# Kernel optimization log

Hardware: AMD Instinct MI355X
Metric: run time of the kernel (lower is better)

The kernel has to match this reference:

```python
import jax, jax.numpy as jnp
import numpy as np

B, T, C, H = 2, 2048, 1024, 16
HD = C // H  # head dim = 64


def setup_inputs() -> dict:
    key = jax.random.key(0)
    ks = jax.random.split(key, 5)
    scale = 0.02
    return {
        "x": jax.random.normal(ks[0], (B, T, C), dtype=jnp.float32),
        "W_attn": jax.random.normal(ks[1], (C, 3 * C), dtype=jnp.float32) * scale,
        "b_attn": jax.random.normal(ks[2], (3 * C,), dtype=jnp.float32) * scale,
        "W_proj": jax.random.normal(ks[3], (C, C), dtype=jnp.float32) * scale,
        "b_proj": jax.random.normal(ks[4], (C,), dtype=jnp.float32) * scale,
    }


def reference(x, W_attn, b_attn, W_proj, b_proj):
    Bd, Td, Cd = x.shape
    qkv = x @ W_attn + b_attn                      # [B,T,3C]
    q, k, v = jnp.split(qkv, 3, axis=-1)           # each [B,T,C]
    # [B,T,C] -> [B,H,T,HD]
    def heads(t):
        return t.reshape(Bd, Td, H, HD).transpose(0, 2, 1, 3)
    q, k, v = heads(q), heads(k), heads(v)
    att = jnp.einsum('bhqd,bhkd->bhqk', q, k) * (1.0 / np.sqrt(HD))
    causal = jnp.tril(jnp.ones((Td, Td), dtype=bool))
    att = jnp.where(causal[None, None, :, :], att, -jnp.inf)
    att = jax.nn.softmax(att, axis=-1)
    y = jnp.einsum('bhqk,bhkd->bhqd', att, v)      # [B,H,T,HD]
    y = y.transpose(0, 2, 1, 3).reshape(Bd, Td, Cd)
    return y @ W_proj + b_proj
```

## Files before the change

### kernel.cpp

```cpp
#include <hip/hip_runtime.h>
#include <hip/hip_bf16.h>


typedef __attribute__((ext_vector_type(8))) __bf16 bf16x8;
typedef __attribute__((ext_vector_type(8))) short short8;
typedef __attribute__((ext_vector_type(4))) short short4v;
typedef __attribute__((ext_vector_type(4))) float floatx4;

__device__ __forceinline__ unsigned short f2b(float f) {
    unsigned int x = __float_as_uint(f);
    x += 0x7fffu + ((x >> 16) & 1u);
    return (unsigned short)(x >> 16);
}
__device__ __forceinline__ unsigned short f2b_trunc(float f) {
    return (unsigned short)(__float_as_uint(f) >> 16);
}
__device__ __forceinline__ void gld16(const void* g, void* l) {
    __builtin_amdgcn_global_load_lds((const __attribute__((address_space(1))) void*)g,
                                     (__attribute__((address_space(3))) void*)l, 16, 0, 0);
}

__global__ __launch_bounds__(256) void cvt_k(
    const float* __restrict__ in, unsigned short* __restrict__ out, int n)
{
    int i = (blockIdx.x * 256 + threadIdx.x) << 3;
    if (i >= n) return;
    const float4 a = *(const float4*)(in + i);
    const float4 b = *(const float4*)(in + i + 4);
    short8 v;
    v[0] = (short)f2b(a.x); v[1] = (short)f2b(a.y);
    v[2] = (short)f2b(a.z); v[3] = (short)f2b(a.w);
    v[4] = (short)f2b(b.x); v[5] = (short)f2b(b.y);
    v[6] = (short)f2b(b.z); v[7] = (short)f2b(b.w);
    *(short8*)(out + i) = v;
}

__global__ __launch_bounds__(256) void transpose_cvt_k(
    const float* __restrict__ in, unsigned short* __restrict__ out,
    int R, int Cc)
{
    __shared__ unsigned short tl[64][72];
    const int t = threadIdx.x;
    const int r0 = blockIdx.y * 64, c0 = blockIdx.x * 64;
#pragma unroll
    for (int it = 0; it < 2; ++it) {
        int idx = it * 256 + t, r = idx >> 3, c8 = (idx & 7) << 3;
        const float* p = in + (size_t)(r0 + r) * Cc + c0 + c8;
        const float4 a = *(const float4*)p;
        const float4 b = *(const float4*)(p + 4);
        tl[r][c8 + 0] = f2b(a.x); tl[r][c8 + 1] = f2b(a.y);
        tl[r][c8 + 2] = f2b(a.z); tl[r][c8 + 3] = f2b(a.w);
        tl[r][c8 + 4] = f2b(b.x); tl[r][c8 + 5] = f2b(b.y);
        tl[r][c8 + 6] = f2b(b.z); tl[r][c8 + 7] = f2b(b.w);
    }
    __syncthreads();
#pragma unroll
    for (int it = 0; it < 2; ++it) {
        int idx = it * 256 + t, rr = idx >> 3, c8 = (idx & 7) << 3;
        short8 v;
#pragma unroll
        for (int i = 0; i < 8; ++i) v[i] = (short)tl[c8 + i][rr];
        *(short8*)(out + (size_t)(c0 + rr) * R + r0 + c8) = v;
    }
}

__global__ __launch_bounds__(256) void gemm_qkv(
    const unsigned short* __restrict__ A,
    const unsigned short* __restrict__ BT,
    const float* __restrict__ bias,
    unsigned short* __restrict__ outqk,
    unsigned short* __restrict__ outvt)
{
    __shared__ unsigned short Ald[128][32];
    __shared__ unsigned short Bld[128][32];
    __shared__ __align__(16) unsigned short Esc[128 * 72];

    const int t = threadIdx.x;
    const int w = t >> 6, lane = t & 63, l15 = lane & 15, quad = lane >> 4;
    const int wr = w >> 1, wc = w & 1;
    const int m0 = blockIdx.y * 128, n0 = blockIdx.x * 128;
    const int K = 1024;

    float bia[4];
#pragma unroll
    for (int j = 0; j < 4; ++j) bia[j] = bias[n0 + wc * 64 + j * 16 + l15];

    floatx4 acc[4][4];
#pragma unroll
    for (int i = 0; i < 4; ++i)
#pragma unroll
        for (int j = 0; j < 4; ++j) acc[i][j] = (floatx4)0.f;

    const int row_s = t >> 2, kg_s = (t & 3) << 3;
    for (int k0 = 0; k0 < K; k0 += 32) {
        __syncthreads();
#pragma unroll
        for (int c = 0; c < 2; ++c) {
            int row = c * 64 + row_s;
            gld16(A  + (size_t)(m0 + row) * K + k0 + kg_s, &Ald[0][0] + (size_t)(c * 256 + w * 64) * 8);
            gld16(BT + (size_t)(n0 + row) * K + k0 + kg_s, &Bld[0][0] + (size_t)(c * 256 + w * 64) * 8);
        }
        __syncthreads();

        bf16x8 af[4], bfr[4];
#pragma unroll
        for (int i = 0; i < 4; ++i) af[i] = *(const bf16x8*)&Ald[wr * 64 + i * 16 + l15][quad * 8];
#pragma unroll
        for (int j = 0; j < 4; ++j) bfr[j] = *(const bf16x8*)&Bld[wc * 64 + j * 16 + l15][quad * 8];
#pragma unroll
        for (int i = 0; i < 4; ++i)
#pragma unroll
            for (int j = 0; j < 4; ++j)
                acc[i][j] = __builtin_amdgcn_mfma_f32_16x16x32_bf16(af[i], bfr[j], acc[i][j], 0, 0, 0);
    }

    const int bb = m0 >> 11, tbase = m0 & 2047;
    if (n0 < 2048) {
        for (int cf = 0; cf < 2; ++cf) {
            __syncthreads();
            if (wc == cf) {
#pragma unroll
                for (int i = 0; i < 4; ++i)
#pragma unroll
                    for (int j = 0; j < 4; ++j)
#pragma unroll
                        for (int r = 0; r < 4; ++r)
                            Esc[(wr * 64 + i * 16 + quad * 4 + r) * 72 + j * 16 + l15] =
                                f2b(acc[i][j][r] + bia[j]);
            }
            __syncthreads();
            const int fb = n0 + cf * 64;
            const int which = fb >> 10, h = (fb & 1023) >> 6;
            const int row = t >> 1, co = (t & 1) << 5;
            const unsigned short* src = Esc + row * 72 + co;
            unsigned short* dst = outqk + (size_t)which * 4194304
                + (((size_t)(bb * 16 + h) * 2048 + tbase + row) * 64 + co);
#pragma unroll
            for (int u = 0; u < 4; ++u)
                *(short8*)(dst + u * 8) = *(const short8*)(src + u * 8);
        }
    } else {
        const int hb = (n0 & 1023) >> 6;
        for (int hf = 0; hf < 2; ++hf) {
            __syncthreads();
            if (wr == hf) {
#pragma unroll
                for (int i = 0; i < 4; ++i)
#pragma unroll
                    for (int j = 0; j < 4; ++j) {
                        short4v pk;
#pragma unroll
                        for (int r = 0; r < 4; ++r) pk[r] = (short)f2b(acc[i][j][r] + bia[j]);
                        *(short4v*)&Esc[(wc * 64 + j * 16 + l15) * 72 + i * 16 + quad * 4] = pk;
                    }
            }
            __syncthreads();
            const int dl = t >> 1, co = (t & 1) << 5;
            const int h = hb + (dl >> 6), d = dl & 63;
            const unsigned short* src = Esc + dl * 72 + co;
            unsigned short* dst = outvt
                + (((size_t)(bb * 16 + h) * 64 + d) * 2048 + tbase + hf * 64 + co);
#pragma unroll
            for (int u = 0; u < 4; ++u)
                *(short8*)(dst + u * 8) = *(const short8*)(src + u * 8);
        }
    }
}

__global__ __launch_bounds__(256) void gemm_proj(
    const unsigned short* __restrict__ A,
    const unsigned short* __restrict__ BT,
    const float* __restrict__ bias,
    float* __restrict__ outf)
{
    __shared__ unsigned short Ald[128][32];
    __shared__ unsigned short Bld[64][32];
    __shared__ __align__(16) float Ef[32 * 68];

    const int t = threadIdx.x;
    const int w = t >> 6, lane = t & 63, l15 = lane & 15, quad = lane >> 4;
    const int m0 = blockIdx.y * 128, n0 = blockIdx.x * 64;
    const int K = 1024, N = 1024;

    float bia[4];
#pragma unroll
    for (int j = 0; j < 4; ++j) bia[j] = bias[n0 + j * 16 + l15];

    floatx4 acc[2][4];
#pragma unroll
    for (int i = 0; i < 2; ++i)
#pragma unroll
        for (int j = 0; j < 4; ++j) acc[i][j] = (floatx4)0.f;

    const int row_s = t >> 2, kg_s = (t & 3) << 3;
    for (int k0 = 0; k0 < K; k0 += 32) {
        __syncthreads();
#pragma unroll
        for (int c = 0; c < 2; ++c)
            gld16(A + (size_t)(m0 + c * 64 + row_s) * K + k0 + kg_s,
                  &Ald[0][0] + (size_t)(c * 256 + w * 64) * 8);
        gld16(BT + (size_t)(n0 + row_s) * K + k0 + kg_s,
              &Bld[0][0] + (size_t)(w * 64) * 8);
        __syncthreads();

        bf16x8 af[2], bfr[4];
#pragma unroll
        for (int i = 0; i < 2; ++i) af[i] = *(const bf16x8*)&Ald[w * 32 + i * 16 + l15][quad * 8];
#pragma unroll
        for (int j = 0; j < 4; ++j) bfr[j] = *(const bf16x8*)&Bld[j * 16 + l15][quad * 8];
#pragma unroll
        for (int i = 0; i < 2; ++i)
#pragma unroll
            for (int j = 0; j < 4; ++j)
                acc[i][j] = __builtin_amdgcn_mfma_f32_16x16x32_bf16(af[i], bfr[j], acc[i][j], 0, 0, 0);
    }

    for (int qf = 0; qf < 4; ++qf) {
        __syncthreads();
        if (w == qf) {
#pragma unroll
            for (int i = 0; i < 2; ++i)
#pragma unroll
                for (int j = 0; j < 4; ++j)
#pragma unroll
                    for (int r = 0; r < 4; ++r)
                        Ef[(i * 16 + quad * 4 + r) * 68 + j * 16 + l15] = acc[i][j][r] + bia[j];
        }
        __syncthreads();
        const int row = t >> 3, co = (t & 7) << 3;
        const float* src = Ef + row * 68 + co;
        float* dst = outf + (size_t)(m0 + qf * 32 + row) * N + n0 + co;
#pragma unroll
        for (int u = 0; u < 2; ++u)
            *(float4*)(dst + u * 4) = *(const float4*)(src + u * 4);
    }
}

__global__ __launch_bounds__(256) void attn_k(
    const unsigned short* __restrict__ qg,
    const unsigned short* __restrict__ kg,
    const unsigned short* __restrict__ vt,
    unsigned short* __restrict__ y)
{
    __shared__ unsigned short Kb[2][64][64];
    __shared__ unsigned short Vb[2][64][64];
    __shared__ unsigned short Pld[4][16][72];

    const int t = threadIdx.x, w = t >> 6, lane = t & 63;
    const int l15 = lane & 15, quad = lane >> 4;
    const int bh = blockIdx.x >> 4, p = blockIdx.x & 15;
    const int b = bh >> 4, h = bh & 15;
    const float SC = 0.18033688011112042f;

    bf16x8 ones;
#pragma unroll
    for (int i = 0; i < 8; ++i) ones[i] = (__bf16)1.0f;

    const int r_s = t >> 3;
    const int g_s = t & 7;

#pragma unroll 1
    for (int hv = 0; hv < 2; ++hv) {
        const int qt = hv ? (31 - p) : p;
        const int qbase = qt * 64;

        bf16x8 qa[2];
        {
            const unsigned short* qrow = qg + ((size_t)bh * 2048 + qbase + w * 16 + l15) * 64;
            qa[0] = *(const bf16x8*)(qrow + quad * 8);
            qa[1] = *(const bf16x8*)(qrow + 32 + quad * 8);
        }

        floatx4 O[4];
#pragma unroll
        for (int j = 0; j < 4; ++j) O[j] = (floatx4)0.f;
        floatx4 lacc = (floatx4)0.f;

        __syncthreads();
        {
#pragma unroll
            for (int c = 0; c < 2; ++c) {
                int r = c * 32 + r_s;
                int cg = (g_s ^ (r & 7)) << 3;
                gld16(kg + ((size_t)bh * 2048 + r) * 64 + cg,
                      &Kb[0][0][0] + (size_t)(c * 256 + w * 64) * 8);
                gld16(vt + ((size_t)bh * 64 + r) * 2048 + cg,
                      &Vb[0][0][0] + (size_t)(c * 256 + w * 64) * 8);
            }
        }

#pragma unroll 1
        for (int kt = 0; kt <= qt; ++kt) {
            __syncthreads();
            const int cur = kt & 1;
            if (kt < qt) {
                const int kbase = (kt + 1) * 64, nxt = cur ^ 1;
#pragma unroll
                for (int c = 0; c < 2; ++c) {
                    int r = c * 32 + r_s;
                    int cg = (g_s ^ (r & 7)) << 3;
                    gld16(kg + ((size_t)bh * 2048 + kbase + r) * 64 + cg,
                          &Kb[nxt][0][0] + (size_t)(c * 256 + w * 64) * 8);
                    gld16(vt + ((size_t)bh * 64 + r) * 2048 + kbase + cg,
                          &Vb[nxt][0][0] + (size_t)(c * 256 + w * 64) * 8);
                }
            }

            floatx4 sv[4];
#pragma unroll
            for (int jn = 0; jn < 4; ++jn) sv[jn] = (floatx4)0.f;
#pragma unroll
            for (int kk = 0; kk < 2; ++kk) {
#pragma unroll
                for (int jn = 0; jn < 4; ++jn) {
                    bf16x8 bfr = *(const bf16x8*)&Kb[cur][jn * 16 + l15][((kk * 4 + quad) ^ (l15 & 7)) << 3];
                    sv[jn] = __builtin_amdgcn_mfma_f32_16x16x32_bf16(qa[kk], bfr, sv[jn], 0, 0, 0);
                }
            }

            if (kt == qt) {
#pragma unroll
                for (int jn = 0; jn < 4; ++jn) {
                    int key = jn * 16 + l15;
#pragma unroll
                    for (int r = 0; r < 4; ++r) {
                        int qr = w * 16 + quad * 4 + r;
                        float s = (key > qr) ? -1e30f : sv[jn][r];
                        sv[jn][r] = exp2f(s * SC);
                    }
                }
            } else {
#pragma unroll
                for (int jn = 0; jn < 4; ++jn)
#pragma unroll
                    for (int r = 0; r < 4; ++r) sv[jn][r] = exp2f(sv[jn][r] * SC);
            }

#pragma unroll
            for (int jn = 0; jn < 4; ++jn)
#pragma unroll
                for (int r = 0; r < 4; ++r)
                    Pld[w][quad * 4 + r][jn * 16 + l15] = f2b_trunc(sv[jn][r]);
            __builtin_amdgcn_wave_barrier();
            __builtin_amdgcn_s_waitcnt(0xc07f);
            __builtin_amdgcn_wave_barrier();

#pragma unroll
            for (int kk = 0; kk < 2; ++kk) {
                bf16x8 pa = *(const bf16x8*)&Pld[w][l15][kk * 32 + quad * 8];
                lacc = __builtin_amdgcn_mfma_f32_16x16x32_bf16(pa, ones, lacc, 0, 0, 0);
#pragma unroll
                for (int jd = 0; jd < 4; ++jd) {
                    bf16x8 vb = *(const bf16x8*)&Vb[cur][jd * 16 + l15][((kk * 4 + quad) ^ (l15 & 7)) << 3];
                    O[jd] = __builtin_amdgcn_mfma_f32_16x16x32_bf16(pa, vb, O[jd], 0, 0, 0);
                }
            }
        }

#pragma unroll
        for (int r = 0; r < 4; ++r) {
            float inv = 1.f / lacc[r];
            int tt = qbase + w * 16 + quad * 4 + r;
#pragma unroll
            for (int jd = 0; jd < 4; ++jd) {
                int c = h * 64 + jd * 16 + l15;
                y[((size_t)b * 2048 + tt) * 1024 + c] = f2b(O[jd][r] * inv);
            }
        }
    }
}

extern "C" void kernel_launch(void* const* d_in, const int* in_sizes, int n_in,
                              void* d_out, int out_size, void* d_ws, size_t ws_size,
                              hipStream_t stream) {
    const float* x      = (const float*)d_in[0];
    const float* W_attn = (const float*)d_in[1];
    const float* b_attn = (const float*)d_in[2];
    const float* W_proj = (const float*)d_in[3];
    const float* b_proj = (const float*)d_in[4];
    float* out = (float*)d_out;

    char* ws = (char*)d_ws;
    unsigned short* qk  = (unsigned short*)(ws);
    unsigned short* vtb = (unsigned short*)(ws + 16777216);
    unsigned short* y   = (unsigned short*)(ws + 25165824);
    unsigned short* xb  = (unsigned short*)(ws + 33554432);
    unsigned short* WTa = (unsigned short*)(ws + 41943040);
    unsigned short* WTp = (unsigned short*)(ws + 48234496);

    cvt_k<<<2048, 256, 0, stream>>>(x, xb, 4194304);
    transpose_cvt_k<<<dim3(48, 16), 256, 0, stream>>>(W_attn, WTa, 1024, 3072);
    transpose_cvt_k<<<dim3(16, 16), 256, 0, stream>>>(W_proj, WTp, 1024, 1024);
    gemm_qkv<<<dim3(24, 32), 256, 0, stream>>>(xb, WTa, b_attn, qk, vtb);
    attn_k<<<512, 256, 0, stream>>>(qk, qk + 4194304, vtb, y);
    gemm_proj<<<dim3(16, 32), 256, 0, stream>>>(y, WTp, b_proj, out);
}
```

Before: 209.3 us.

## Double-buffer LDS in both GEMMs and widen projection tile to 128x128

Both GEMM kernels now use two LDS buffers. The next K-slice is fetched with global_load_lds while MFMAs run on the current one, and one of the two barriers per iteration is dropped. The projection GEMM also moves from 128x64 to 128x128 tiles with a 2x2 wave layout, so each block does more reuse per load but the grid shrinks to 256 blocks. The epilogue scratch is aliased onto the double buffer to limit LDS use. The main risk is the single-barrier scheme: it relies on the async LDS writes having completed before the next barrier without an explicit vmcnt wait.

```diff
diff --git a/kernel.cpp b/kernel.cpp
--- a/kernel.cpp
+++ b/kernel.cpp
@@ -71,9 +71,8 @@
     unsigned short* __restrict__ outqk,
     unsigned short* __restrict__ outvt)
 {
-    __shared__ unsigned short Ald[128][32];
-    __shared__ unsigned short Bld[128][32];
-    __shared__ __align__(16) unsigned short Esc[128 * 72];
+    __shared__ __align__(16) unsigned short SM[2][2][128][32];
+    unsigned short* Esc = &SM[0][0][0][0];
 
     const int t = threadIdx.x;
     const int w = t >> 6, lane = t & 63, l15 = lane & 15, quad = lane >> 4;
@@ -92,21 +91,32 @@
         for (int j = 0; j < 4; ++j) acc[i][j] = (floatx4)0.f;
 
     const int row_s = t >> 2, kg_s = (t & 3) << 3;
-    for (int k0 = 0; k0 < K; k0 += 32) {
+    const unsigned short* gA = A  + (size_t)(m0 + row_s) * K + kg_s;
+    const unsigned short* gB = BT + (size_t)(n0 + row_s) * K + kg_s;
+    const int ldst = (w * 64) * 8;
+
+#pragma unroll
+    for (int c = 0; c < 2; ++c) {
+        gld16(gA + (size_t)c * 64 * K, &SM[0][0][0][0] + c * 2048 + ldst);
+        gld16(gB + (size_t)c * 64 * K, &SM[0][1][0][0] + c * 2048 + ldst);
+    }
+
+    for (int it = 0; it < 32; ++it) {
         __syncthreads();
-#pragma unroll
-        for (int c = 0; c < 2; ++c) {
-            int row = c * 64 + row_s;
-            gld16(A  + (size_t)(m0 + row) * K + k0 + kg_s, &Ald[0][0] + (size_t)(c * 256 + w * 64) * 8);
-            gld16(BT + (size_t)(n0 + row) * K + k0 + kg_s, &Bld[0][0] + (size_t)(c * 256 + w * 64) * 8);
-        }
-        __syncthreads();
-
+        const int cur = it & 1;
+        if (it < 31) {
+            const int k0 = (it + 1) * 32;
+#pragma unroll
+            for (int c = 0; c < 2; ++c) {
+                gld16(gA + (size_t)c * 64 * K + k0, &SM[cur ^ 1][0][0][0] + c * 2048 + ldst);
+                gld16(gB + (size_t)c * 64 * K + k0, &SM[cur ^ 1][1][0][0] + c * 2048 + ldst);
+            }
+        }
         bf16x8 af[4], bfr[4];
 #pragma unroll
-        for (int i = 0; i < 4; ++i) af[i] = *(const bf16x8*)&Ald[wr * 64 + i * 16 + l15][quad * 8];
-#pragma unroll
-        for (int j = 0; j < 4; ++j) bfr[j] = *(const bf16x8*)&Bld[wc * 64 + j * 16 + l15][quad * 8];
+        for (int i = 0; i < 4; ++i) af[i] = *(const bf16x8*)&SM[cur][0][wr * 64 + i * 16 + l15][quad * 8];
+#pragma unroll
+        for (int j = 0; j < 4; ++j) bfr[j] = *(const bf16x8*)&SM[cur][1][wc * 64 + j * 16 + l15][quad * 8];
 #pragma unroll
         for (int i = 0; i < 4; ++i)
 #pragma unroll
@@ -173,43 +183,54 @@
     const float* __restrict__ bias,
     float* __restrict__ outf)
 {
-    __shared__ unsigned short Ald[128][32];
-    __shared__ unsigned short Bld[64][32];
-    __shared__ __align__(16) float Ef[32 * 68];
+    __shared__ __align__(16) unsigned short SM[2][2][128][32];
+    float* Ef = (float*)&SM[0][0][0][0];
 
     const int t = threadIdx.x;
     const int w = t >> 6, lane = t & 63, l15 = lane & 15, quad = lane >> 4;
-    const int m0 = blockIdx.y * 128, n0 = blockIdx.x * 64;
+    const int wr = w >> 1, wc = w & 1;
+    const int m0 = blockIdx.y * 128, n0 = blockIdx.x * 128;
     const int K = 1024, N = 1024;
 
     float bia[4];
 #pragma unroll
-    for (int j = 0; j < 4; ++j) bia[j] = bias[n0 + j * 16 + l15];
-
-    floatx4 acc[2][4];
-#pragma unroll
-    for (int i = 0; i < 2; ++i)
+    for (int j = 0; j < 4; ++j) bia[j] = bias[n0 + wc * 64 + j * 16 + l15];
+
+    floatx4 acc[4][4];
+#pragma unroll
+    for (int i = 0; i < 4; ++i)
 #pragma unroll
         for (int j = 0; j < 4; ++j) acc[i][j] = (floatx4)0.f;
 
     const int row_s = t >> 2, kg_s = (t & 3) << 3;
-    for (int k0 = 0; k0 < K; k0 += 32) {
+    const unsigned short* gA = A  + (size_t)(m0 + row_s) * K + kg_s;
+    const unsigned short* gB = BT + (size_t)(n0 + row_s) * K + kg_s;
+    const int ldst = (w * 64) * 8;
+
+#pragma unroll
+    for (int c = 0; c < 2; ++c) {
+        gld16(gA + (size_t)c * 64 * K, &SM[0][0][0][0] + c * 2048 + ldst);
+        gld16(gB + (size_t)c * 64 * K, &SM[0][1][0][0] + c * 2048 + ldst);
+    }
+
+    for (int it = 0; it < 32; ++it) {
         __syncthreads();
-#pragma unroll
-        for (int c = 0; c < 2; ++c)
-            gld16(A + (size_t)(m0 + c * 64 + row_s) * K + k0 + kg_s,
-                  &Ald[0][0] + (size_t)(c * 256 + w * 64) * 8);
-        gld16(BT + (size_t)(n0 + row_s) * K + k0 + kg_s,
-              &Bld[0][0] + (size_t)(w * 64) * 8);
-        __syncthreads();
-
-        bf16x8 af[2], bfr[4];
-#pragma unroll
-        for (int i = 0; i < 2; ++i) af[i] = *(const bf16x8*)&Ald[w * 32 + i * 16 + l15][quad * 8];
-#pragma unroll
-        for (int j = 0; j < 4; ++j) bfr[j] = *(const bf16x8*)&Bld[j * 16 + l15][quad * 8];
-#pragma unroll
-        for (int i = 0; i < 2; ++i)
+        const int cur = it & 1;
+        if (it < 31) {
+            const int k0 = (it + 1) * 32;
+#pragma unroll
+            for (int c = 0; c < 2; ++c) {
+                gld16(gA + (size_t)c * 64 * K + k0, &SM[cur ^ 1][0][0][0] + c * 2048 + ldst);
+                gld16(gB + (size_t)c * 64 * K + k0, &SM[cur ^ 1][1][0][0] + c * 2048 + ldst);
+            }
+        }
+        bf16x8 af[4], bfr[4];
+#pragma unroll
+        for (int i = 0; i < 4; ++i) af[i] = *(const bf16x8*)&SM[cur][0][wr * 64 + i * 16 + l15][quad * 8];
+#pragma unroll
+        for (int j = 0; j < 4; ++j) bfr[j] = *(const bf16x8*)&SM[cur][1][wc * 64 + j * 16 + l15][quad * 8];
+#pragma unroll
+        for (int i = 0; i < 4; ++i)
 #pragma unroll
             for (int j = 0; j < 4; ++j)
                 acc[i][j] = __builtin_amdgcn_mfma_f32_16x16x32_bf16(af[i], bfr[j], acc[i][j], 0, 0, 0);
@@ -217,21 +238,23 @@
 
     for (int qf = 0; qf < 4; ++qf) {
         __syncthreads();
-        if (w == qf) {
-#pragma unroll
-            for (int i = 0; i < 2; ++i)
+        if (wr == (qf >> 1)) {
+            const int ib = (qf & 1) * 2;
+#pragma unroll
+            for (int ii = 0; ii < 2; ++ii)
 #pragma unroll
                 for (int j = 0; j < 4; ++j)
 #pragma unroll
                     for (int r = 0; r < 4; ++r)
-                        Ef[(i * 16 + quad * 4 + r) * 68 + j * 16 + l15] = acc[i][j][r] + bia[j];
+                        Ef[(ii * 16 + quad * 4 + r) * 132 + wc * 64 + j * 16 + l15] =
+                            acc[ib + ii][j][r] + bia[j];
         }
         __syncthreads();
-        const int row = t >> 3, co = (t & 7) << 3;
-        const float* src = Ef + row * 68 + co;
+        const int row = t >> 3, co = (t & 7) << 4;
+        const float* src = Ef + row * 132 + co;
         float* dst = outf + (size_t)(m0 + qf * 32 + row) * N + n0 + co;
 #pragma unroll
-        for (int u = 0; u < 2; ++u)
+        for (int u = 0; u < 4; ++u)
             *(float4*)(dst + u * 4) = *(const float4*)(src + u * 4);
     }
 }
@@ -393,5 +416,5 @@
     transpose_cvt_k<<<dim3(16, 16), 256, 0, stream>>>(W_proj, WTp, 1024, 1024);
     gemm_qkv<<<dim3(24, 32), 256, 0, stream>>>(xb, WTa, b_attn, qk, vtb);
     attn_k<<<512, 256, 0, stream>>>(qk, qk + 4194304, vtb, y);
-    gemm_proj<<<dim3(16, 32), 256, 0, stream>>>(y, WTp, b_proj, out);
-}
+    gemm_proj<<<dim3(8, 32), 256, 0, stream>>>(y, WTp, b_proj, out);
+}
```

Result: faster. 203.7 us (-2.7%).
